# Performance work log

Hardware: AMD Instinct MI355X
Metric: run time of the kernel (lower is better)

Reference implementation:

```python
import jax, jax.numpy as jnp
import numpy as np

B, S, I, H, O, L = 32, 512, 128, 1024, 128, 3


def setup_inputs() -> dict:
    key = jax.random.key(0)
    ks = jax.random.split(key, 22)
    si = 1.0 / np.sqrt(I)
    sh = 1.0 / np.sqrt(H)
    f32 = jnp.float32
    d = {}
    d['x'] = jax.random.normal(ks[0], (B, S, I), f32)
    # layer 0 (input dim I)
    d['Wxz0'] = jax.random.normal(ks[1], (H, I), f32) * si
    d['Whz0'] = jax.random.normal(ks[2], (H, H), f32) * sh
    d['bz0'] = jax.random.normal(ks[3], (H,), f32) * sh
    d['Wxr0'] = jax.random.normal(ks[4], (H, I), f32) * si
    d['Whr0'] = jax.random.normal(ks[5], (H, H), f32) * sh
    d['br0'] = jax.random.normal(ks[6], (H,), f32) * sh
    d['Wxg0'] = jax.random.normal(ks[7], (H, I), f32) * si
    d['Whg0'] = jax.random.normal(ks[8], (H, H), f32) * sh
    d['bg0'] = jax.random.normal(ks[9], (H,), f32) * sh
    # layers 1..L-1 stacked (input dim H)
    Lm1 = L - 1
    d['Wxz'] = jax.random.normal(ks[10], (Lm1, H, H), f32) * sh
    d['Whz'] = jax.random.normal(ks[11], (Lm1, H, H), f32) * sh
    d['bz'] = jax.random.normal(ks[12], (Lm1, H), f32) * sh
    d['Wxr'] = jax.random.normal(ks[13], (Lm1, H, H), f32) * sh
    d['Whr'] = jax.random.normal(ks[14], (Lm1, H, H), f32) * sh
    d['br'] = jax.random.normal(ks[15], (Lm1, H), f32) * sh
    d['Wxg'] = jax.random.normal(ks[16], (Lm1, H, H), f32) * sh
    d['Whg'] = jax.random.normal(ks[17], (Lm1, H, H), f32) * sh
    d['bg'] = jax.random.normal(ks[18], (Lm1, H), f32) * sh
    # output head
    d['Wout'] = jax.random.normal(ks[19], (O, H), f32) * sh
    d['bout'] = jax.random.normal(ks[20], (O,), f32) * sh
    return d


def _gru_cell(x, h, Wx_z, Wh_z, b_z, Wx_r, Wh_r, b_r, Wx_g, Wh_g, b_g):
    # x: (B, in), h: (B, H); torch Linear convention y = x @ W.T + b
    z = jax.nn.sigmoid(x @ Wx_z.T + h @ Wh_z.T + b_z)
    r = jax.nn.sigmoid(x @ Wx_r.T + h @ Wh_r.T + b_r)
    g = jnp.tanh(x @ Wx_g.T + (r * h) @ Wh_g.T + b_g)
    return z * h + (1.0 - z) * g


def reference(x, Wxz0, Whz0, bz0, Wxr0, Whr0, br0, Wxg0, Whg0, bg0,
              Wxz, Whz, bz, Wxr, Whr, br, Wxg, Whg, bg, Wout, bout):
    Bsz = x.shape[0]
    Hd = Whz0.shape[0]
    Lm1 = Wxz.shape[0]
    n_layers = Lm1 + 1

    def step(hs, x_t):
        # hs: (L, B, H); x_t: (B, I)
        h0 = _gru_cell(x_t, hs[0], Wxz0, Whz0, bz0, Wxr0, Whr0, br0, Wxg0, Whg0, bg0)
        new = [h0]
        inp = h0  # dropout=0 -> identity between layers
        for k in range(Lm1):
            hk = _gru_cell(inp, hs[k + 1], Wxz[k], Whz[k], bz[k], Wxr[k], Whr[k], br[k], Wxg[k], Whg[k], bg[k])
            new.append(hk)
            inp = hk
        out_t = inp @ Wout.T + bout  # (B, O)
        return jnp.stack(new), out_t

    h_init = jnp.zeros((n_layers, Bsz, Hd), dtype=x.dtype)
    hs_final, outs = jax.lax.scan(step, h_init, jnp.swapaxes(x, 0, 1))
    layer_output = jnp.swapaxes(outs, 0, 1)      # (B, S, O)
    hidden_state = jnp.swapaxes(hs_final, 0, 1)  # (B, L, H)
    return layer_output, hidden_state
```

## Files before the change

kernel.cpp:

```cpp
#include <hip/hip_runtime.h>


#ifndef __has_builtin
#define __has_builtin(x) 0
#endif
#if __has_builtin(__builtin_amdgcn_fdot2_f32_bf16)
#define HAS_DOT2 1
typedef __bf16 bf16x2 __attribute__((ext_vector_type(2)));
#else
#define HAS_DOT2 0
#endif

struct GruParams {
  const float* x;
  const float* Wx[3][3];
  const float* Wh[3][3];
  const float* bias[3][3];
  const float* Wout;
  const float* bout;
  unsigned* hP;
  unsigned* rhP;
  float* hF;
  unsigned* bar;
  float* out;
  float* outHid;
};

#define WH0z 0
#define WH0r 2048
#define WH0g 4096
#define WH1z 6144
#define WH1r 8192
#define WH1g 10240
#define WH2z 12288
#define WH2r 14336
#define WH2g 16384
#define WX1z 18432
#define WX1r 20480
#define WX1g 22528
#define WX2z 24576
#define WX2r 26624
#define WX2g 28672
#define WOUTO 30720
#define SCRO  31232
#define LDSB ((SCRO + 8 * 1184) * 4)

extern __shared__ unsigned lds_u[];

__device__ __forceinline__ unsigned loadcu(const unsigned* p_) {
  return __hip_atomic_load(p_, __ATOMIC_RELAXED, __HIP_MEMORY_SCOPE_AGENT);
}
__device__ __forceinline__ void storecu(unsigned* p_, unsigned v) {
  __hip_atomic_store(p_, v, __ATOMIC_RELAXED, __HIP_MEMORY_SCOPE_AGENT);
}

__device__ __forceinline__ unsigned short f2bfu(float f) {
  union { float f; unsigned u; } c; c.f = f;
  unsigned r = c.u + 0x7fffu + ((c.u >> 16) & 1u);
  return (unsigned short)(r >> 16);
}
__device__ __forceinline__ unsigned pack2(float f0, float f1) {
  return ((unsigned)f2bfu(f1) << 16) | (unsigned)f2bfu(f0);
}

__device__ __forceinline__ float d2(float acc, unsigned a, unsigned w) {
#if HAS_DOT2
  return __builtin_amdgcn_fdot2_f32_bf16(__builtin_bit_cast(bf16x2, a),
                                         __builtin_bit_cast(bf16x2, w),
                                         acc, false);
#else
  union { unsigned u; float f; } al, ah, wl, wh;
  al.u = a << 16; ah.u = a & 0xffff0000u;
  wl.u = w << 16; wh.u = w & 0xffff0000u;
  return acc + al.f * wl.f + ah.f * wh.f;
#endif
}
__device__ __forceinline__ float d8(float acc, unsigned a0, unsigned a1,
                                    unsigned a2, unsigned a3, const uint4 wv) {
  return d2(d2(d2(d2(acc, a0, wv.x), a1, wv.y), a2, wv.z), a3, wv.w);
}
__device__ __forceinline__ void fma4(float& acc, float o0, float o1, float o2,
                                     float o3, const float4 v) {
  acc += o0 * v.x; acc += o1 * v.y; acc += o2 * v.z; acc += o3 * v.w;
}

__device__ __forceinline__ void gridbar(unsigned* bar, unsigned phase, int bid) {
  __syncthreads();
  if (threadIdx.x == 0) {
    const int g = bid & 15;
    unsigned* grp   = bar + (g << 5);
    unsigned* root  = bar + 512;
    unsigned* go    = bar + 544;
    unsigned* grpGo = bar + 576 + (g << 5);
    const unsigned tgt = phase << 4;
    unsigned old = __hip_atomic_fetch_add(grp, 1u, __ATOMIC_RELAXED, __HIP_MEMORY_SCOPE_AGENT);
    if (old == tgt - 1u) {
      unsigned r = __hip_atomic_fetch_add(root, 1u, __ATOMIC_RELAXED, __HIP_MEMORY_SCOPE_AGENT);
      if (r == tgt - 1u)
        __hip_atomic_store(go, phase, __ATOMIC_RELAXED, __HIP_MEMORY_SCOPE_AGENT);
      while (__hip_atomic_load(go, __ATOMIC_RELAXED, __HIP_MEMORY_SCOPE_AGENT) < phase)
        __builtin_amdgcn_s_sleep(2);
      __hip_atomic_store(grpGo, phase, __ATOMIC_RELAXED, __HIP_MEMORY_SCOPE_AGENT);
    } else {
      while (__hip_atomic_load(grpGo, __ATOMIC_RELAXED, __HIP_MEMORY_SCOPE_AGENT) < phase)
        __builtin_amdgcn_s_sleep(2);
    }
  }
  __syncthreads();
}

__global__ __launch_bounds__(512, 2) void gruPersist(GruParams p) {
  const int tid   = threadIdx.x;
  const int bid   = blockIdx.x;
  const int wPhys = tid >> 6;
  const int w     = (wPhys + bid) & 7;
  const int lane  = tid & 63;
  const int b     = lane & 31;
  const int ks    = lane >> 5;
  const int jbase = bid << 2;
  float* scratch = (float*)(lds_u + SCRO);
  float* slot    = scratch + wPhys * 1184;

  for (int d = tid; d < 15 * 2048; d += 512) {
    const int s = d >> 11, rem = d & 2047;
    const int jj = rem >> 9, kp = rem & 511;
    const float* src;
    if (s < 9)       src = p.Wh[s / 3][s % 3];
    else if (s < 12) src = p.Wx[1][s - 9];
    else             src = p.Wx[2][s - 12];
    const size_t base = (size_t)(jbase + jj) * 1024 + (size_t)(kp << 1);
    lds_u[d] = pack2(src[base], src[base + 1]);
  }
  if (bid < 128) {
    const size_t base = (size_t)bid * 1024 + (size_t)(tid << 1);
    lds_u[WOUTO + tid] = pack2(p.Wout[base], p.Wout[base + 1]);
  }
  __syncthreads();

  unsigned* hP0 = p.hP;            unsigned* hP1 = p.hP + 16384;
  unsigned* hP2 = p.hP + 32768;
  unsigned* rq0 = p.rhP;           unsigned* rq1 = p.rhP + 16384;
  unsigned* rq2 = p.rhP + 32768;

  const int sboff = ((w << 6) + (ks << 2)) * 32 + b;
  const unsigned* pA0 = hP0 + sboff;
  const unsigned* pA1 = hP1 + sboff;
  const unsigned* pA2 = hP2 + sboff;
  const unsigned* pR0 = rq0 + sboff;
  const unsigned* pR1 = rq1 + sboff;
  const unsigned* pR2 = rq2 + sboff;

  const int el  = tid >> 6;
  const int ejp = (tid & 63) >> 5, ebb = tid & 31;
  const int ej0 = jbase + (ejp << 1);
  float hPrev[2] = {0.f, 0.f};
  float bZ[2], bR[2], bG[2];
  if (tid < 192) {
    #pragma unroll
    for (int q = 0; q < 2; ++q) {
      bZ[q] = p.bias[el][0][ej0 + q];
      bR[q] = p.bias[el][1][ej0 + q];
      bG[q] = p.bias[el][2][ej0 + q];
    }
  }
  float boutv = 0.f;
  if (bid < 128 && tid < 32) boutv = p.bout[bid];

  unsigned phase = 0;
  float myZ[2] = {0.f, 0.f}, myGx[2] = {0.f, 0.f};

  float xz[4]={0,0,0,0}, xr[4]={0,0,0,0}, xg[4]={0,0,0,0};
  {
    const float* xb = p.x + ((size_t)b << 16);
    #pragma unroll
    for (int i = 0; i < 2; ++i) {
      const int k = (w << 4) + (i << 3) + (ks << 2);
      const float4 xv = *(const float4*)(xb + k);
      #pragma unroll
      for (int jj = 0; jj < 4; ++jj) {
        const size_t row = (size_t)(jbase + jj) * 128 + k;
        fma4(xz[jj], xv.x,xv.y,xv.z,xv.w, *(const float4*)(p.Wx[0][0] + row));
        fma4(xr[jj], xv.x,xv.y,xv.z,xv.w, *(const float4*)(p.Wx[0][1] + row));
        fma4(xg[jj], xv.x,xv.y,xv.z,xv.w, *(const float4*)(p.Wx[0][2] + row));
      }
    }
  }

  for (int m = 0; m < 514; ++m) {
    const bool act0 = (m < 512);
    const bool act1 = (m >= 1 && m <= 512);
    const bool act2 = (m >= 2 && m <= 513);
    const int t0 = m, t1 = m - 1, t2 = m - 2, th = m - 3;

    float a0z[4], a0r[4], a0g[4];
    float a1z[4]={0,0,0,0}, a1r[4]={0,0,0,0}, a1g[4]={0,0,0,0};
    float a2z[4]={0,0,0,0}, a2r[4]={0,0,0,0}, a2g[4]={0,0,0,0};
    float ah = 0.f;
    #pragma unroll
    for (int jj = 0; jj < 4; ++jj) { a0z[jj]=xz[jj]; a0r[jj]=xr[jj]; a0g[jj]=xg[jj]; }

    #pragma unroll 2
    for (int i = 0; i < 8; ++i) {
      const int kp0 = (w << 6) + (i << 3) + (ks << 2);
      const unsigned a0 = loadcu(pA0 + i*256 + 0);
      const unsigned a1 = loadcu(pA0 + i*256 + 32);
      const unsigned a2 = loadcu(pA0 + i*256 + 64);
      const unsigned a3 = loadcu(pA0 + i*256 + 96);
      #pragma unroll
      for (int jj = 0; jj < 4; ++jj) {
        const int wo = (jj << 9) + kp0;
        a0z[jj] = d8(a0z[jj], a0,a1,a2,a3, *(const uint4*)(lds_u + WH0z + wo));
        a0r[jj] = d8(a0r[jj], a0,a1,a2,a3, *(const uint4*)(lds_u + WH0r + wo));
        a1z[jj] = d8(a1z[jj], a0,a1,a2,a3, *(const uint4*)(lds_u + WX1z + wo));
        a1r[jj] = d8(a1r[jj], a0,a1,a2,a3, *(const uint4*)(lds_u + WX1r + wo));
        a1g[jj] = d8(a1g[jj], a0,a1,a2,a3, *(const uint4*)(lds_u + WX1g + wo));
      }
    }

    #pragma unroll 2
    for (int i = 0; i < 8; ++i) {
      const int kp0 = (w << 6) + (i << 3) + (ks << 2);
      const unsigned a0 = loadcu(pA1 + i*256 + 0);
      const unsigned a1 = loadcu(pA1 + i*256 + 32);
      const unsigned a2 = loadcu(pA1 + i*256 + 64);
      const unsigned a3 = loadcu(pA1 + i*256 + 96);
      #pragma unroll
      for (int jj = 0; jj < 4; ++jj) {
        const int wo = (jj << 9) + kp0;
        a1z[jj] = d8(a1z[jj], a0,a1,a2,a3, *(const uint4*)(lds_u + WH1z + wo));
        a1r[jj] = d8(a1r[jj], a0,a1,a2,a3, *(const uint4*)(lds_u + WH1r + wo));
        a2z[jj] = d8(a2z[jj], a0,a1,a2,a3, *(const uint4*)(lds_u + WX2z + wo));
        a2r[jj] = d8(a2r[jj], a0,a1,a2,a3, *(const uint4*)(lds_u + WX2r + wo));
        a2g[jj] = d8(a2g[jj], a0,a1,a2,a3, *(const uint4*)(lds_u + WX2g + wo));
      }
    }

    #pragma unroll 2
    for (int i = 0; i < 8; ++i) {
      const int kp0 = (w << 6) + (i << 3) + (ks << 2);
      const unsigned a0 = loadcu(pA2 + i*256 + 0);
      const unsigned a1 = loadcu(pA2 + i*256 + 32);
      const unsigned a2 = loadcu(pA2 + i*256 + 64);
      const unsigned a3 = loadcu(pA2 + i*256 + 96);
      #pragma unroll
      for (int jj = 0; jj < 4; ++jj) {
        const int wo = (jj << 9) + kp0;
        a2z[jj] = d8(a2z[jj], a0,a1,a2,a3, *(const uint4*)(lds_u + WH2z + wo));
        a2r[jj] = d8(a2r[jj], a0,a1,a2,a3, *(const uint4*)(lds_u + WH2r + wo));
      }
      if (bid < 128)
        ah = d8(ah, a0,a1,a2,a3, *(const uint4*)(lds_u + WOUTO + kp0));
    }

    #pragma unroll
    for (int jj = 0; jj < 4; ++jj) {
      a0z[jj] += __shfl_xor(a0z[jj], 32);
      a0r[jj] += __shfl_xor(a0r[jj], 32);
      a0g[jj] += __shfl_xor(a0g[jj], 32);
      a1z[jj] += __shfl_xor(a1z[jj], 32);
      a1r[jj] += __shfl_xor(a1r[jj], 32);
      a1g[jj] += __shfl_xor(a1g[jj], 32);
      a2z[jj] += __shfl_xor(a2z[jj], 32);
      a2r[jj] += __shfl_xor(a2r[jj], 32);
      a2g[jj] += __shfl_xor(a2g[jj], 32);
    }
    ah += __shfl_xor(ah, 32);

    if (ks == 0) {
      #pragma unroll
      for (int jj = 0; jj < 4; ++jj) {
        slot[(0*4+jj)*32 + b] = a0z[jj];
        slot[(1*4+jj)*32 + b] = a0r[jj];
        slot[(2*4+jj)*32 + b] = a0g[jj];
        slot[(3*4+jj)*32 + b] = a1z[jj];
        slot[(4*4+jj)*32 + b] = a1r[jj];
        slot[(5*4+jj)*32 + b] = a1g[jj];
        slot[(6*4+jj)*32 + b] = a2z[jj];
        slot[(7*4+jj)*32 + b] = a2r[jj];
        slot[(8*4+jj)*32 + b] = a2g[jj];
      }
      slot[1152 + b] = ah;
    }
    __syncthreads();

    if (tid < 192) {
      float rr0 = 0.f, rr1 = 0.f;
      #pragma unroll
      for (int q = 0; q < 2; ++q) {
        const int jj = (ejp << 1) + q;
        float sz = 0.f, sr = 0.f, sg = 0.f;
        #pragma unroll
        for (int ww = 0; ww < 8; ++ww) {
          sz += scratch[ww * 1184 + ((el*3+0)*4 + jj)*32 + ebb];
          sr += scratch[ww * 1184 + ((el*3+1)*4 + jj)*32 + ebb];
          sg += scratch[ww * 1184 + ((el*3+2)*4 + jj)*32 + ebb];
        }
        const float zp = sz + bZ[q];
        const float rp = sr + bR[q];
        myGx[q] = sg + bG[q];
        myZ[q]  = 1.f / (1.f + expf(-zp));
        const float r = 1.f / (1.f + expf(-rp));
        const float rrv = r * hPrev[q];
        if (q) rr1 = rrv; else rr0 = rrv;
      }
      unsigned* rq = (el == 0) ? rq0 : (el == 1) ? rq1 : rq2;
      storecu(rq + ((bid << 1) + ejp) * 32 + ebb, pack2(rr0, rr1));
    }
    if (m >= 3 && bid < 128 && tid < 32) {
      float s = 0.f;
      #pragma unroll
      for (int ww = 0; ww < 8; ++ww) s += scratch[ww * 1184 + 1152 + tid];
      p.out[((size_t)tid << 16) + ((size_t)th << 7) + bid] = s + boutv;
    }

    ++phase; gridbar(p.bar, phase, bid);

    float c0[4]={0,0,0,0}, c1[4]={0,0,0,0}, c2[4]={0,0,0,0};
    #pragma unroll 2
    for (int i = 0; i < 8; ++i) {
      const int kp0 = (w << 6) + (i << 3) + (ks << 2);
      const unsigned q00 = loadcu(pR0 + i*256 + 0);
      const unsigned q01 = loadcu(pR0 + i*256 + 32);
      const unsigned q02 = loadcu(pR0 + i*256 + 64);
      const unsigned q03 = loadcu(pR0 + i*256 + 96);
      const unsigned q10 = loadcu(pR1 + i*256 + 0);
      const unsigned q11 = loadcu(pR1 + i*256 + 32);
      const unsigned q12 = loadcu(pR1 + i*256 + 64);
      const unsigned q13 = loadcu(pR1 + i*256 + 96);
      const unsigned q20 = loadcu(pR2 + i*256 + 0);
      const unsigned q21 = loadcu(pR2 + i*256 + 32);
      const unsigned q22 = loadcu(pR2 + i*256 + 64);
      const unsigned q23 = loadcu(pR2 + i*256 + 96);
      #pragma unroll
      for (int jj = 0; jj < 4; ++jj) {
        const int wo = (jj << 9) + kp0;
        c0[jj] = d8(c0[jj], q00,q01,q02,q03, *(const uint4*)(lds_u + WH0g + wo));
        c1[jj] = d8(c1[jj], q10,q11,q12,q13, *(const uint4*)(lds_u + WH1g + wo));
        c2[jj] = d8(c2[jj], q20,q21,q22,q23, *(const uint4*)(lds_u + WH2g + wo));
      }
    }
    #pragma unroll
    for (int jj = 0; jj < 4; ++jj) {
      c0[jj] += __shfl_xor(c0[jj], 32);
      c1[jj] += __shfl_xor(c1[jj], 32);
      c2[jj] += __shfl_xor(c2[jj], 32);
    }
    if (ks == 0) {
      #pragma unroll
      for (int jj = 0; jj < 4; ++jj) {
        slot[(0*4+jj)*32 + b] = c0[jj];
        slot[(1*4+jj)*32 + b] = c1[jj];
        slot[(2*4+jj)*32 + b] = c2[jj];
      }
    }
    __syncthreads();
    if (tid < 192) {
      const bool act = (el == 0) ? act0 : (el == 1) ? act1 : act2;
      if (act) {
        const int tl = (el == 0) ? t0 : (el == 1) ? t1 : t2;
        #pragma unroll
        for (int q = 0; q < 2; ++q) {
          const int jj = (ejp << 1) + q;
          float cv = 0.f;
          #pragma unroll
          for (int ww = 0; ww < 8; ++ww)
            cv += scratch[ww * 1184 + (el*4 + jj)*32 + ebb];
          const float g = tanhf(cv + myGx[q]);
          const float hn = myZ[q] * hPrev[q] + (1.f - myZ[q]) * g;
          hPrev[q] = hn;
          if (tl == 511) p.outHid[ebb * 3072 + el * 1024 + (ej0 + q)] = hn;
        }
        unsigned* hq = (el == 0) ? hP0 : (el == 1) ? hP1 : hP2;
        storecu(hq + ((bid << 1) + ejp) * 32 + ebb, pack2(hPrev[0], hPrev[1]));
      }
    }

    #pragma unroll
    for (int jj = 0; jj < 4; ++jj) { xz[jj]=0.f; xr[jj]=0.f; xg[jj]=0.f; }
    if (m + 1 < 512) {
      const float* xb = p.x + ((size_t)b << 16) + ((size_t)(m + 1) << 7);
      #pragma unroll
      for (int i = 0; i < 2; ++i) {
        const int k = (w << 4) + (i << 3) + (ks << 2);
        const float4 xv = *(const float4*)(xb + k);
        #pragma unroll
        for (int jj = 0; jj < 4; ++jj) {
          const size_t row = (size_t)(jbase + jj) * 128 + k;
          fma4(xz[jj], xv.x,xv.y,xv.z,xv.w, *(const float4*)(p.Wx[0][0] + row));
          fma4(xr[jj], xv.x,xv.y,xv.z,xv.w, *(const float4*)(p.Wx[0][1] + row));
          fma4(xg[jj], xv.x,xv.y,xv.z,xv.w, *(const float4*)(p.Wx[0][2] + row));
        }
      }
    }

    ++phase; gridbar(p.bar, phase, bid);
  }

  float ah = 0.f;
  if (bid < 128) {
    #pragma unroll 2
    for (int i = 0; i < 8; ++i) {
      const int kp0 = (w << 6) + (i << 3) + (ks << 2);
      const unsigned a0 = loadcu(pA2 + i*256 + 0);
      const unsigned a1 = loadcu(pA2 + i*256 + 32);
      const unsigned a2 = loadcu(pA2 + i*256 + 64);
      const unsigned a3 = loadcu(pA2 + i*256 + 96);
      ah = d8(ah, a0,a1,a2,a3, *(const uint4*)(lds_u + WOUTO + kp0));
    }
    ah += __shfl_xor(ah, 32);
    if (ks == 0) scratch[wPhys * 64 + b] = ah;
  }
  __syncthreads();
  if (bid < 128 && tid < 32) {
    float s = 0.f;
    #pragma unroll
    for (int ww = 0; ww < 8; ++ww) s += scratch[ww * 64 + tid];
    p.out[((size_t)tid << 16) + ((size_t)511 << 7) + bid] = s + boutv;
  }
}

__global__ void initWs(unsigned* wsd) {
  const int i = blockIdx.x * 1024 + threadIdx.x;
  if (i < 198656) wsd[i] = 0u;
}

extern "C" void kernel_launch(void* const* d_in, const int* in_sizes, int n_in,
                              void* d_out, int out_size, void* d_ws, size_t ws_size,
                              hipStream_t stream)
{
  GruParams P;
  P.x = (const float*)d_in[0];
  P.Wx[0][0] = (const float*)d_in[1];  P.Wh[0][0] = (const float*)d_in[2];
  P.bias[0][0] = (const float*)d_in[3];
  P.Wx[0][1] = (const float*)d_in[4];  P.Wh[0][1] = (const float*)d_in[5];
  P.bias[0][1] = (const float*)d_in[6];
  P.Wx[0][2] = (const float*)d_in[7];  P.Wh[0][2] = (const float*)d_in[8];
  P.bias[0][2] = (const float*)d_in[9];
  for (int l = 1; l < 3; ++l) {
    const size_t off = (size_t)(l - 1) * 1048576;
    const size_t ob  = (size_t)(l - 1) * 1024;
    P.Wx[l][0] = (const float*)d_in[10] + off; P.Wh[l][0] = (const float*)d_in[11] + off;
    P.bias[l][0] = (const float*)d_in[12] + ob;
    P.Wx[l][1] = (const float*)d_in[13] + off; P.Wh[l][1] = (const float*)d_in[14] + off;
    P.bias[l][1] = (const float*)d_in[15] + ob;
    P.Wx[l][2] = (const float*)d_in[16] + off; P.Wh[l][2] = (const float*)d_in[17] + off;
    P.bias[l][2] = (const float*)d_in[18] + ob;
  }
  P.Wout = (const float*)d_in[19];
  P.bout = (const float*)d_in[20];

  char* ws = (char*)d_ws;
  P.hP  = (unsigned*)ws;
  P.rhP = (unsigned*)(ws + 196608);
  P.hF  = (float*)(ws + 393216);
  P.bar = (unsigned*)(ws + 786432);
  P.out = (float*)d_out;
  P.outHid = P.out + 2097152;

  hipFuncSetAttribute(reinterpret_cast<const void*>(gruPersist),
                      hipFuncAttributeMaxDynamicSharedMemorySize, LDSB);

  initWs<<<194, 1024, 0, stream>>>((unsigned*)ws);
  gruPersist<<<256, 512, LDSB, stream>>>(P);
}
```

Measured before the change: 15.38 ms.

## Replace grid-wide barriers with per-wave group counters for fine-grained dependencies

Replaces the two hierarchical grid barriers per timestep with per-group arrival counters: each block signals its 32-block group after finishing a phase, and each wave waits only on the group that produced the hidden-state slice it reads. This turns a full all-to-all barrier into point-to-point dependency waits, letting waves start as soon as their own inputs are ready. It adds more spinning atomics per wave and relies on relaxed ordering being sufficient for visibility of the cache-bypassing stores.

After: 17.34 ms. +12.7%, slower.

```diff
diff --git a/kernel.cpp b/kernel.cpp
--- a/kernel.cpp
+++ b/kernel.cpp
@@ -84,29 +84,12 @@
   acc += o0 * v.x; acc += o1 * v.y; acc += o2 * v.z; acc += o3 * v.w;
 }
 
-__device__ __forceinline__ void gridbar(unsigned* bar, unsigned phase, int bid) {
-  __syncthreads();
-  if (threadIdx.x == 0) {
-    const int g = bid & 15;
-    unsigned* grp   = bar + (g << 5);
-    unsigned* root  = bar + 512;
-    unsigned* go    = bar + 544;
-    unsigned* grpGo = bar + 576 + (g << 5);
-    const unsigned tgt = phase << 4;
-    unsigned old = __hip_atomic_fetch_add(grp, 1u, __ATOMIC_RELAXED, __HIP_MEMORY_SCOPE_AGENT);
-    if (old == tgt - 1u) {
-      unsigned r = __hip_atomic_fetch_add(root, 1u, __ATOMIC_RELAXED, __HIP_MEMORY_SCOPE_AGENT);
-      if (r == tgt - 1u)
-        __hip_atomic_store(go, phase, __ATOMIC_RELAXED, __HIP_MEMORY_SCOPE_AGENT);
-      while (__hip_atomic_load(go, __ATOMIC_RELAXED, __HIP_MEMORY_SCOPE_AGENT) < phase)
-        __builtin_amdgcn_s_sleep(2);
-      __hip_atomic_store(grpGo, phase, __ATOMIC_RELAXED, __HIP_MEMORY_SCOPE_AGENT);
-    } else {
-      while (__hip_atomic_load(grpGo, __ATOMIC_RELAXED, __HIP_MEMORY_SCOPE_AGENT) < phase)
-        __builtin_amdgcn_s_sleep(2);
-    }
-  }
-  __syncthreads();
+__device__ __forceinline__ void groupArrive(unsigned* ctr) {
+  __hip_atomic_fetch_add(ctr, 1u, __ATOMIC_RELAXED, __HIP_MEMORY_SCOPE_AGENT);
+}
+__device__ __forceinline__ void groupWait(const unsigned* ctr, unsigned tgt) {
+  while (__hip_atomic_load(ctr, __ATOMIC_RELAXED, __HIP_MEMORY_SCOPE_AGENT) < tgt)
+    __builtin_amdgcn_s_sleep(2);
 }
 
 __global__ __launch_bounds__(512, 2) void gruPersist(GruParams p) {
@@ -118,6 +101,7 @@
   const int b     = lane & 31;
   const int ks    = lane >> 5;
   const int jbase = bid << 2;
+  const int grp   = bid >> 5;
   float* scratch = (float*)(lds_u + SCRO);
   float* slot    = scratch + wPhys * 1184;
 
@@ -141,6 +125,8 @@
   unsigned* hP2 = p.hP + 32768;
   unsigned* rq0 = p.rhP;           unsigned* rq1 = p.rhP + 16384;
   unsigned* rq2 = p.rhP + 32768;
+  unsigned* arr1 = p.bar;
+  unsigned* arr2 = p.bar + 256;
 
   const int sboff = ((w << 6) + (ks << 2)) * 32 + b;
   const unsigned* pA0 = hP0 + sboff;
@@ -166,7 +152,6 @@
   float boutv = 0.f;
   if (bid < 128 && tid < 32) boutv = p.bout[bid];
 
-  unsigned phase = 0;
   float myZ[2] = {0.f, 0.f}, myGx[2] = {0.f, 0.f};
 
   float xz[4]={0,0,0,0}, xr[4]={0,0,0,0}, xg[4]={0,0,0,0};
@@ -198,6 +183,8 @@
     float ah = 0.f;
     #pragma unroll
     for (int jj = 0; jj < 4; ++jj) { a0z[jj]=xz[jj]; a0r[jj]=xr[jj]; a0g[jj]=xg[jj]; }
+
+    groupWait(arr2 + (w << 5), 32u * (unsigned)m);
 
     #pragma unroll 2
     for (int i = 0; i < 8; ++i) {
@@ -312,8 +299,10 @@
       for (int ww = 0; ww < 8; ++ww) s += scratch[ww * 1184 + 1152 + tid];
       p.out[((size_t)tid << 16) + ((size_t)th << 7) + bid] = s + boutv;
     }
-
-    ++phase; gridbar(p.bar, phase, bid);
+    __syncthreads();
+    if (tid == 0) groupArrive(arr1 + (grp << 5));
+
+    groupWait(arr1 + (w << 5), 32u * (unsigned)(m + 1));
 
     float c0[4]={0,0,0,0}, c1[4]={0,0,0,0}, c2[4]={0,0,0,0};
     #pragma unroll 2
@@ -393,11 +382,13 @@
       }
     }
 
-    ++phase; gridbar(p.bar, phase, bid);
+    __syncthreads();
+    if (tid == 0) groupArrive(arr2 + (grp << 5));
   }
 
   float ah = 0.f;
   if (bid < 128) {
+    groupWait(arr2 + (w << 5), 32u * 514u);
     #pragma unroll 2
     for (int i = 0; i < 8; ++i) {
       const int kp0 = (w << 6) + (i << 3) + (ks << 2);
```
